# Kernel tuning notes

Hardware: AMD Instinct MI355X
Metric: run time of the kernel (lower is better)

Reference implementation:

```python
import jax, jax.numpy as jnp
import numpy as np
from jax import lax

DIM = 128
HEADS = 4
HEAD_DIM = DIM // HEADS          # 32
SR = 2
BN_EPS = 1e-5


def setup_inputs() -> dict:
    key = jax.random.key(0)
    ks = jax.random.split(key, 16)
    B, N, C = 8, 3136, DIM
    H = W = 56
    Nkv = (H // SR) * (W // SR)  # 784
    s = 0.05
    inp = {
        "x": jax.random.normal(ks[0], (B, N, C), jnp.float32),
        "relative_pos": jax.random.normal(ks[1], (HEADS, N, Nkv), jnp.float32),
        "Wq": jax.random.normal(ks[2], (C, C), jnp.float32) * s,
        "bq": jnp.zeros((C,), jnp.float32),
        "Wk": jax.random.normal(ks[3], (C, C), jnp.float32) * s,
        "bk": jnp.zeros((C,), jnp.float32),
        "Wv": jax.random.normal(ks[4], (C, C), jnp.float32) * s,
        "bv": jnp.zeros((C,), jnp.float32),
        "conv_w": jax.random.normal(ks[5], (C, 1, SR, SR), jnp.float32) * s,  # depthwise OIHW
        "conv_b": jnp.zeros((C,), jnp.float32),
        "bn_gamma": jnp.ones((C,), jnp.float32),
        "bn_beta": jnp.zeros((C,), jnp.float32),
        "bn_mean": jax.random.normal(ks[6], (C,), jnp.float32) * 0.1,
        "bn_var": jax.random.uniform(ks[7], (C,), jnp.float32, 0.5, 1.5),
        "Wp": jax.random.normal(ks[8], (C, C), jnp.float32) * s,
        "bp": jnp.zeros((C,), jnp.float32),
        "H": H,
        "W": W,
    }
    return inp


def reference(x, relative_pos, Wq, bq, Wk, bk, Wv, bv, conv_w, conv_b,
              bn_gamma, bn_beta, bn_mean, bn_var, Wp, bp, H, W):
    B, N, C = x.shape
    scale = HEAD_DIM ** -0.5

    # q: (B, heads, N, head_dim)
    q = (x @ Wq + bq).reshape(B, N, HEADS, HEAD_DIM).transpose(0, 2, 1, 3)

    # spatial reduction: depthwise conv stride SR + BatchNorm (eval, running stats)
    x_img = x.transpose(0, 2, 1).reshape(B, C, H, W)
    y = lax.conv_general_dilated(
        x_img, conv_w, window_strides=(SR, SR), padding="VALID",
        feature_group_count=C,
        dimension_numbers=("NCHW", "OIHW", "NCHW")) + conv_b[None, :, None, None]
    inv = bn_gamma * lax.rsqrt(bn_var + BN_EPS)
    y = y * inv[None, :, None, None] + (bn_beta - bn_mean * inv)[None, :, None, None]
    x_ = y.reshape(B, C, -1).transpose(0, 2, 1)  # (B, Nkv, C)
    Nkv = x_.shape[1]

    k = (x_ @ Wk + bk).reshape(B, Nkv, HEADS, HEAD_DIM).transpose(0, 2, 1, 3)
    v = (x_ @ Wv + bv).reshape(B, Nkv, HEADS, HEAD_DIM).transpose(0, 2, 1, 3)

    attn = jnp.einsum("bhnd,bhmd->bhnm", q, k) * scale + relative_pos[None]
    attn = jax.nn.softmax(attn, axis=-1)
    out = jnp.einsum("bhnm,bhmd->bhnd", attn, v)
    out = out.transpose(0, 2, 1, 3).reshape(B, N, C)
    return out @ Wp + bp
```

## Files before the change

kernel.cpp:

```cpp
#include <hip/hip_runtime.h>
#include <hip/hip_bf16.h>

#define BATCH 8
#define NQ 3136
#define CDIM 128
#define NHEAD 4
#define HD 32
#define NKV 784
#define HIMG 56
#define SCALE 0.17677669529663687f

typedef __attribute__((ext_vector_type(8))) short bf8_t;
typedef __attribute__((ext_vector_type(4))) float f4_t;

using bf16 = __hip_bfloat16;
using u16  = unsigned short;

static __device__ __forceinline__ float b2f(bf16 v){ return __bfloat162float(v); }
static __device__ __forceinline__ bf16  f2b(float v){ return __float2bfloat16(v); }
static __device__ __forceinline__ short f2s(float v){
  union { bf16 b; short s; } u; u.b = f2b(v); return u.s;
}
static __device__ __forceinline__ float u16f(u16 x){
  union { u16 u; bf16 b; } c; c.u = x; return b2f(c.b);
}
static __device__ __forceinline__ float ld1(const void* p, size_t i, int f){
  return f ? b2f(((const bf16*)p)[i]) : ((const float*)p)[i];
}
static __device__ __forceinline__ float4 ld4f(const void* p, size_t i, int f){
  if (f){
    ushort4 u = *(const ushort4*)((const bf16*)p + i);
    return make_float4(u16f(u.x), u16f(u.y), u16f(u.z), u16f(u.w));
  }
  return *(const float4*)((const float*)p + i);
}
static __device__ __forceinline__ bf8_t ld8(const void* p, size_t i, int f){
  if (f) return *(const bf8_t*)((const bf16*)p + i);
  const float* fp = (const float*)p + i;
  float4 a = *(const float4*)fp;
  float4 b = *(const float4*)(fp + 4);
  bf8_t r;
  r[0]=f2s(a.x); r[1]=f2s(a.y); r[2]=f2s(a.z); r[3]=f2s(a.w);
  r[4]=f2s(b.x); r[5]=f2s(b.y); r[6]=f2s(b.z); r[7]=f2s(b.w);
  return r;
}
static __device__ __forceinline__ int detect_flag(const void* var_raw){
  const u16* h = (const u16*)var_raw;
  int lane = threadIdx.x & 63;
  bool ok = true;
  #pragma unroll
  for (int t = 0; t < 2; t++){
    union { u16 u; bf16 b; } cv; cv.u = h[lane + 64*t];
    float v = b2f(cv.b);
    ok = ok && (v > 0.3f) && (v < 1.7f);
  }
  return (__ballot(ok) == ~0ull) ? 1 : 0;
}

static __device__ __forceinline__ void mfma_row(
    const bf8_t a[4], const bf16* __restrict__ Wt, int m, int g, f4_t acc[8])
{
  #pragma unroll
  for (int ct = 0; ct < 8; ct++){
    f4_t c = {0.f,0.f,0.f,0.f};
    const bf16* bp = Wt + (size_t)(ct*16 + m)*CDIM + 8*g;
    #pragma unroll
    for (int ks = 0; ks < 4; ks++){
      bf8_t b = *(const bf8_t*)(bp + 32*ks);
      c = __builtin_amdgcn_mfma_f32_16x16x32_bf16(a[ks], b, c, 0,0,0);
    }
    acc[ct] = c;
  }
}

__global__ __launch_bounds__(256) void prep_kernel(
    const void* __restrict__ Wq, const void* __restrict__ Wk,
    const void* __restrict__ Wv, const void* __restrict__ Wp,
    const void* __restrict__ var, const void* __restrict__ cw,
    const void* __restrict__ cb, const void* __restrict__ gam,
    const void* __restrict__ bet, const void* __restrict__ mea,
    const void* __restrict__ bq, const void* __restrict__ bk,
    const void* __restrict__ bv, const void* __restrict__ bp,
    bf16* __restrict__ Wqt, bf16* __restrict__ Wkt,
    bf16* __restrict__ Wvt, bf16* __restrict__ Wpt,
    bf16* __restrict__ bqs, bf16* __restrict__ bks,
    bf16* __restrict__ bvs, bf16* __restrict__ bps,
    float* __restrict__ cwf, float* __restrict__ inv, float* __restrict__ shift2)
{
  int f = detect_flag(var);
  int idx = blockIdx.x*256 + threadIdx.x;
  int mat = idx >> 14;
  int e   = idx & 16383;
  int o = e >> 7, i = e & 127;
  const void* src; bf16* dst; float s = 1.f;
  if      (mat == 0){ src = Wq; dst = Wqt; s = SCALE; }
  else if (mat == 1){ src = Wk; dst = Wkt; }
  else if (mat == 2){ src = Wv; dst = Wvt; }
  else              { src = Wp; dst = Wpt; }
  dst[e] = f2b(ld1(src, (size_t)i*128 + o, f) * s);

  if (blockIdx.x == 0){
    int t = threadIdx.x;
    { int e2 = t;       cwf[(e2&3)*128 + (e2>>2)] = ld1(cw, e2, f); }
    { int e2 = t + 256; cwf[(e2&3)*128 + (e2>>2)] = ld1(cw, e2, f); }
    if (t < 128){
      bqs[t] = f2b(ld1(bq, t, f) * SCALE);
      bks[t] = f2b(ld1(bk, t, f));
      bvs[t] = f2b(ld1(bv, t, f));
      bps[t] = f2b(ld1(bp, t, f));
      float iv = ld1(gam, t, f) * rsqrtf(ld1(var, t, f) + 1e-5f);
      inv[t] = iv;
      shift2[t] = ld1(bet, t, f) - ld1(mea, t, f) * iv + ld1(cb, t, f) * iv;
    }
  }
}

__global__ __launch_bounds__(256) void fat_kernel(
    const void* __restrict__ x, const void* __restrict__ var,
    const float* __restrict__ cwf, const float* __restrict__ inv,
    const float* __restrict__ shift2, bf16* __restrict__ xr,
    const bf16* __restrict__ Wqt, const bf16* __restrict__ bqs,
    bf16* __restrict__ qbf,
    const void* __restrict__ rel, bf16* __restrict__ relb, int qblk)
{
  int f = detect_flag(var);
  if (blockIdx.x < 784){
    int idx = blockIdx.x*256 + threadIdx.x;
    int c0 = (idx & 31)*4;
    int t  = idx >> 5;
    int b  = t / NKV;
    int kv = t - b*NKV;
    int i = kv/28, j = kv - i*28;
    size_t base = (size_t)(b*NQ + 2*i*HIMG + 2*j)*CDIM + c0;
    float4 t0 = ld4f(x, base, f);
    float4 t1 = ld4f(x, base + CDIM, f);
    float4 t2 = ld4f(x, base + HIMG*CDIM, f);
    float4 t3 = ld4f(x, base + HIMG*CDIM + CDIM, f);
    float4 w0 = *(const float4*)(cwf + c0);
    float4 w1 = *(const float4*)(cwf + 128 + c0);
    float4 w2 = *(const float4*)(cwf + 256 + c0);
    float4 w3 = *(const float4*)(cwf + 384 + c0);
    float4 iv4 = *(const float4*)(inv + c0);
    float4 sh4 = *(const float4*)(shift2 + c0);
    union { u16 h[4]; uint2 u; } pk;
    float a;
    a = t0.x*w0.x + t1.x*w1.x + t2.x*w2.x + t3.x*w3.x; pk.h[0] = (u16)f2s(a*iv4.x + sh4.x);
    a = t0.y*w0.y + t1.y*w1.y + t2.y*w2.y + t3.y*w3.y; pk.h[1] = (u16)f2s(a*iv4.y + sh4.y);
    a = t0.z*w0.z + t1.z*w1.z + t2.z*w2.z + t3.z*w3.z; pk.h[2] = (u16)f2s(a*iv4.z + sh4.z);
    a = t0.w*w0.w + t1.w*w1.w + t2.w*w2.w + t3.w*w3.w; pk.h[3] = (u16)f2s(a*iv4.w + sh4.w);
    *(uint2*)(xr + (size_t)t*CDIM + c0) = pk.u;
  } else if ((int)blockIdx.x < 784 + qblk){
    int wave = threadIdx.x >> 6, lane = threadIdx.x & 63;
    int m = lane & 15, g = lane >> 4;
    int task = (blockIdx.x - 784)*4 + wave;
    int row0 = task*16;
    bf8_t a[4];
    #pragma unroll
    for (int ks = 0; ks < 4; ks++)
      a[ks] = ld8(x, (size_t)(row0 + m)*CDIM + 8*g + 32*ks, f);
    f4_t acc[8];
    mfma_row(a, Wqt, m, g, acc);
    #pragma unroll
    for (int ct = 0; ct < 8; ct++){
      int col = ct*16 + m;
      float bv = b2f(bqs[col]);
      #pragma unroll
      for (int r = 0; r < 4; r++)
        qbf[(size_t)(row0 + 4*g + r)*CDIM + col] = f2b(acc[ct][r] + bv);
    }
  } else {
    if (f) return;
    int bi = blockIdx.x - 784 - qblk;
    size_t gid = ((size_t)bi*256 + threadIdx.x)*8;
    const float* fp = (const float*)rel + gid;
    float4 a  = *(const float4*)fp;
    float4 b4 = *(const float4*)(fp + 4);
    union { u16 hh[8]; uint4 u4; } pk;
    pk.hh[0]=(u16)f2s(a.x);  pk.hh[1]=(u16)f2s(a.y);
    pk.hh[2]=(u16)f2s(a.z);  pk.hh[3]=(u16)f2s(a.w);
    pk.hh[4]=(u16)f2s(b4.x); pk.hh[5]=(u16)f2s(b4.y);
    pk.hh[6]=(u16)f2s(b4.z); pk.hh[7]=(u16)f2s(b4.w);
    *(uint4*)(relb + gid) = pk.u4;
  }
}

__global__ __launch_bounds__(256) void kv_kernel(
    const bf16* __restrict__ xr,
    const bf16* __restrict__ Wkt, const bf16* __restrict__ Wvt,
    const bf16* __restrict__ bks, const bf16* __restrict__ bvs,
    bf16* __restrict__ kbf, bf16* __restrict__ vtb)
{
  int wave = threadIdx.x >> 6, lane = threadIdx.x & 63;
  int m = lane & 15, g = lane >> 4;
  bool isK = blockIdx.x < 98;
  int bx = isK ? blockIdx.x : blockIdx.x - 98;
  int row0 = (bx*4 + wave)*16;
  bf8_t a[4];
  #pragma unroll
  for (int ks = 0; ks < 4; ks++)
    a[ks] = *(const bf8_t*)(xr + (size_t)(row0 + m)*CDIM + 8*g + 32*ks);
  f4_t acc[8];
  mfma_row(a, isK ? Wkt : Wvt, m, g, acc);

  if (isK){
    #pragma unroll
    for (int ct = 0; ct < 8; ct++){
      int col = ct*16 + m;
      float bv = b2f(bks[col]);
      #pragma unroll
      for (int r = 0; r < 4; r++)
        kbf[(size_t)(row0 + 4*g + r)*CDIM + col] = f2b(acc[ct][r] + bv);
    }
  } else {
    int b   = row0 / NKV;
    int kv0 = row0 - b*NKV + 4*g;
    #pragma unroll
    for (int ct = 0; ct < 8; ct++){
      int col = ct*16 + m;
      float bv = b2f(bvs[col]);
      int h = col >> 5, d = col & 31;
      union { bf16 hh[4]; uint2 u; } pk;
      #pragma unroll
      for (int r = 0; r < 4; r++) pk.hh[r] = f2b(acc[ct][r] + bv);
      *(uint2*)(vtb + (size_t)((b*NHEAD + h)*HD + d)*NKV + kv0) = pk.u;
    }
  }
}

template<int RM> struct RelV { using T = float4; };
template<> struct RelV<1> { using T = uint2; };

template<int RM>
static __device__ __forceinline__ typename RelV<RM>::T relld(const void* relp, int off){
  if constexpr (RM == 1) return *(const uint2*)((const bf16*)relp + off);
  else                   return *(const float4*)((const float*)relp + off);
}
template<int RM>
static __device__ __forceinline__ float relget(const typename RelV<RM>::T& v, int r){
  if constexpr (RM == 1){
    union { uint2 u; u16 h[4]; } c; c.u = v;
    return u16f(c.h[r]);
  } else {
    return r == 0 ? v.x : (r == 1 ? v.y : (r == 2 ? v.z : v.w));
  }
}
template<int RM>
static __device__ __forceinline__ void ldrel4(
    typename RelV<RM>::T rl[4], const void* relp, int off){
  #pragma unroll
  for (int t = 0; t < 4; t++) rl[t] = relld<RM>(relp, off + 16*t);
}

template<int RM>
static __device__ __forceinline__ void chunk64(
    int kv0, const typename RelV<RM>::T rl[4],
    const bf16* __restrict__ kbase, const bf16* __restrict__ vb0,
    const bf16* __restrict__ vb1, bf16* __restrict__ pl, int m, int g,
    bf8_t q8, float& m_run, float& l_run, f4_t& O0, f4_t& O1)
{
  f4_t s[4];
  #pragma unroll
  for (int t = 0; t < 4; t++){
    bf8_t k8 = *(const bf8_t*)(kbase + (size_t)(kv0 + t*16)*CDIM);
    f4_t z = {0.f,0.f,0.f,0.f};
    s[t] = __builtin_amdgcn_mfma_f32_16x16x32_bf16(k8, q8, z, 0,0,0);
  }
  #pragma unroll
  for (int t = 0; t < 4; t++)
    #pragma unroll
    for (int r = 0; r < 4; r++)
      s[t][r] += relget<RM>(rl[t], r);
  float vmax = s[0][0];
  #pragma unroll
  for (int t = 0; t < 4; t++)
    #pragma unroll
    for (int r = 0; r < 4; r++)
      if (t + r > 0) vmax = fmaxf(vmax, s[t][r]);
  vmax = fmaxf(vmax, __shfl_xor(vmax, 16, 64));
  vmax = fmaxf(vmax, __shfl_xor(vmax, 32, 64));
  float mn = fmaxf(m_run, vmax);
  float al = __expf(m_run - mn);
  m_run = mn;
  l_run *= al;
  #pragma unroll
  for (int r = 0; r < 4; r++){ O0[r] *= al; O1[r] *= al; }
  float lsum = 0.f;
  #pragma unroll
  for (int t = 0; t < 4; t++){
    union { u16 h[4]; uint2 u; } pk;
    #pragma unroll
    for (int r = 0; r < 4; r++){
      float p = __expf(s[t][r] - m_run);
      lsum += p;
      pk.h[r] = (u16)f2s(p);
    }
    *(uint2*)(pl + m*136 + t*16 + 4*g) = pk.u;
  }
  l_run += lsum;
  #pragma unroll
  for (int ks = 0; ks < 2; ks++){
    bf8_t a8 = *(const bf8_t*)(pl + m*136 + ks*32 + 8*g);
    bf8_t v0 = *(const bf8_t*)(vb0 + kv0 + ks*32 + 8*g);
    bf8_t v1 = *(const bf8_t*)(vb1 + kv0 + ks*32 + 8*g);
    O0 = __builtin_amdgcn_mfma_f32_16x16x32_bf16(v0, a8, O0, 0,0,0);
    O1 = __builtin_amdgcn_mfma_f32_16x16x32_bf16(v1, a8, O1, 0,0,0);
  }
}

template<int RM>
static __device__ __forceinline__ void attn_run(
    const void* __restrict__ relp, const bf16* __restrict__ kbase,
    const bf16* __restrict__ vb0, const bf16* __restrict__ vb1,
    bf16* __restrict__ pl, int m, int g,
    bf8_t q8, float& m_run, float& l_run, f4_t& O0, f4_t& O1)
{
  using RT = typename RelV<RM>::T;
  RT rlA[4], rlB[4], rtv;
  ldrel4<RM>(rlA, relp, 4*g);
  #pragma unroll 1
  for (int c2 = 0; c2 < 6; c2++){
    int kv0 = c2*128;
    ldrel4<RM>(rlB, relp, kv0 + 64 + 4*g);
    chunk64<RM>(kv0, rlA, kbase, vb0, vb1, pl, m, g, q8, m_run, l_run, O0, O1);
    if (c2 < 5) ldrel4<RM>(rlA, relp, kv0 + 128 + 4*g);
    else        rtv = relld<RM>(relp, 768 + 4*g);
    chunk64<RM>(kv0 + 64, rlB, kbase, vb0, vb1, pl, m, g, q8, m_run, l_run, O0, O1);
  }
  {
    bf8_t k8 = *(const bf8_t*)(kbase + (size_t)768*CDIM);
    f4_t z = {0.f,0.f,0.f,0.f};
    f4_t s1 = __builtin_amdgcn_mfma_f32_16x16x32_bf16(k8, q8, z, 0,0,0);
    #pragma unroll
    for (int r = 0; r < 4; r++) s1[r] += relget<RM>(rtv, r);
    float vmax = fmaxf(fmaxf(s1[0], s1[1]), fmaxf(s1[2], s1[3]));
    vmax = fmaxf(vmax, __shfl_xor(vmax, 16, 64));
    vmax = fmaxf(vmax, __shfl_xor(vmax, 32, 64));
    float mn = fmaxf(m_run, vmax);
    float al = __expf(m_run - mn);
    m_run = mn;
    l_run *= al;
    #pragma unroll
    for (int r = 0; r < 4; r++){ O0[r] *= al; O1[r] *= al; }
    union { u16 h[4]; uint2 u; } pk;
    float lsum = 0.f;
    #pragma unroll
    for (int r = 0; r < 4; r++){
      float p = __expf(s1[r] - m_run);
      lsum += p;
      pk.h[r] = (u16)f2s(p);
    }
    *(uint2*)(pl + m*136 + 4*g) = pk.u;
    l_run += lsum;
    bf8_t a8, v0, v1;
    if (g >= 2){
      bf8_t z8 = {0,0,0,0,0,0,0,0};
      a8 = z8; v0 = z8; v1 = z8;
    } else {
      a8 = *(const bf8_t*)(pl + m*136 + 8*g);
      v0 = *(const bf8_t*)(vb0 + 768 + 8*g);
      v1 = *(const bf8_t*)(vb1 + 768 + 8*g);
    }
    O0 = __builtin_amdgcn_mfma_f32_16x16x32_bf16(v0, a8, O0, 0,0,0);
    O1 = __builtin_amdgcn_mfma_f32_16x16x32_bf16(v1, a8, O1, 0,0,0);
  }
}

template<int QF, int FB>
static __device__ __forceinline__ void attn_device(
    const bf16* __restrict__ qbf, const void* __restrict__ x,
    const bf16* __restrict__ Wqt, const bf16* __restrict__ bqs,
    const bf16* __restrict__ kb, const bf16* __restrict__ vtb,
    const void* __restrict__ rel, const bf16* __restrict__ relb,
    const void* __restrict__ var,
    void* __restrict__ dout, bf16* __restrict__ obf)
{
  int f = detect_flag(var);
  int wave = threadIdx.x >> 6, lane = threadIdx.x & 63;
  int m = lane & 15, g = lane >> 4;
  int qt = blockIdx.x, h = blockIdx.y, b = blockIdx.z;
  int qrow0 = qt*64 + wave*16;

  __shared__ bf16 Plds[4][16*136];
  bf16* pl = Plds[wave];

  bf8_t q8;
  if constexpr (QF == 0){
    q8 = *(const bf8_t*)(qbf + (size_t)(b*NQ + qrow0 + m)*CDIM + h*HD + 8*g);
  } else {
    bf8_t xa[4];
    #pragma unroll
    for (int ks = 0; ks < 4; ks++)
      xa[ks] = ld8(x, (size_t)(b*NQ + qrow0 + m)*CDIM + 8*g + 32*ks, f);
    f4_t qc0 = {0.f,0.f,0.f,0.f}, qc1 = {0.f,0.f,0.f,0.f};
    const bf16* wp0 = Wqt + (size_t)(h*HD + m)*CDIM + 8*g;
    const bf16* wp1 = Wqt + (size_t)(h*HD + 16 + m)*CDIM + 8*g;
    #pragma unroll
    for (int ks = 0; ks < 4; ks++){
      bf8_t w0 = *(const bf8_t*)(wp0 + 32*ks);
      bf8_t w1 = *(const bf8_t*)(wp1 + 32*ks);
      qc0 = __builtin_amdgcn_mfma_f32_16x16x32_bf16(xa[ks], w0, qc0, 0,0,0);
      qc1 = __builtin_amdgcn_mfma_f32_16x16x32_bf16(xa[ks], w1, qc1, 0,0,0);
    }
    float bv0 = b2f(bqs[h*HD + m]);
    float bv1 = b2f(bqs[h*HD + 16 + m]);
    #pragma unroll
    for (int r = 0; r < 4; r++){
      pl[(4*g + r)*136 + m]      = f2b(qc0[r] + bv0);
      pl[(4*g + r)*136 + 16 + m] = f2b(qc1[r] + bv1);
    }
    q8 = *(const bf8_t*)(pl + m*136 + 8*g);
  }

  const bf16* kbase = kb  + (size_t)(b*NKV + m)*CDIM + h*HD + 8*g;
  const bf16* vb0   = vtb + (size_t)((b*NHEAD + h)*HD + m)*NKV;
  const bf16* vb1   = vtb + (size_t)((b*NHEAD + h)*HD + 16 + m)*NKV;
  size_t rrow = ((size_t)h*NQ + qrow0 + m)*(size_t)NKV;

  float m_run = -1e30f, l_run = 0.f;
  f4_t O0 = {0.f,0.f,0.f,0.f}, O1 = {0.f,0.f,0.f,0.f};

  if constexpr (FB == 0){
    const void* rsrc = f ? (const void*)((const bf16*)rel + rrow)
                         : (const void*)(relb + rrow);
    attn_run<1>(rsrc, kbase, vb0, vb1, pl, m, g, q8, m_run, l_run, O0, O1);
  } else {
    if (f) attn_run<1>((const void*)((const bf16*)rel + rrow), kbase, vb0, vb1,
                       pl, m, g, q8, m_run, l_run, O0, O1);
    else   attn_run<0>((const void*)((const float*)rel + rrow), kbase, vb0, vb1,
                       pl, m, g, q8, m_run, l_run, O0, O1);
  }

  l_run += __shfl_xor(l_run, 16, 64);
  l_run += __shfl_xor(l_run, 32, 64);
  float iv = 1.0f / l_run;

  bf16* ob = (f ? (bf16*)dout : obf)
           + (size_t)(b*NQ + qrow0 + m)*CDIM + h*HD;
  union { u16 h4[4]; uint2 u; } o0, o1;
  #pragma unroll
  for (int r = 0; r < 4; r++){
    o0.h4[r] = (u16)f2s(O0[r] * iv);
    o1.h4[r] = (u16)f2s(O1[r] * iv);
  }
  *(uint2*)(ob + 4*g)      = o0.u;
  *(uint2*)(ob + 16 + 4*g) = o1.u;
}

template<int QF>
__global__ __launch_bounds__(256, 6) void attn_kernel(
    const bf16* __restrict__ qbf, const void* __restrict__ x,
    const bf16* __restrict__ Wqt, const bf16* __restrict__ bqs,
    const bf16* __restrict__ kb, const bf16* __restrict__ vtb,
    const void* __restrict__ rel, const bf16* __restrict__ relb,
    const void* __restrict__ var,
    void* __restrict__ dout, bf16* __restrict__ obf)
{
  attn_device<QF,0>(qbf, x, Wqt, bqs, kb, vtb, rel, relb, var, dout, obf);
}

__global__ __launch_bounds__(256) void attn_kernel_fb(
    const bf16* __restrict__ qbf, const void* __restrict__ x,
    const bf16* __restrict__ Wqt, const bf16* __restrict__ bqs,
    const bf16* __restrict__ kb, const bf16* __restrict__ vtb,
    const void* __restrict__ rel, const bf16* __restrict__ relb,
    const void* __restrict__ var,
    void* __restrict__ dout, bf16* __restrict__ obf)
{
  attn_device<1,1>(qbf, x, Wqt, bqs, kb, vtb, rel, relb, var, dout, obf);
}

__global__ __launch_bounds__(256) void proj_kernel(
    const bf16* A0, const bf16* A1, const bf16* __restrict__ Wt,
    const bf16* __restrict__ bias, void* outp, const void* __restrict__ var)
{
  int f = detect_flag(var);
  const bf16* A = f ? A0 : A1;
  int wave = threadIdx.x >> 6, lane = threadIdx.x & 63;
  int m = lane & 15, g = lane >> 4;
  int row0 = (blockIdx.x*4 + wave)*16;
  bf8_t a[4];
  #pragma unroll
  for (int ks = 0; ks < 4; ks++)
    a[ks] = *(const bf8_t*)(A + (size_t)(row0 + m)*CDIM + 8*g + 32*ks);
  f4_t acc[8];
  mfma_row(a, Wt, m, g, acc);
  #pragma unroll
  for (int ct = 0; ct < 8; ct++){
    int col = ct*16 + m;
    float bv = b2f(bias[col]);
    #pragma unroll
    for (int r = 0; r < 4; r++){
      size_t oi = (size_t)(row0 + 4*g + r)*CDIM + col;
      float v = acc[ct][r] + bv;
      if (f) ((bf16*)outp)[oi]  = f2b(v);
      else   ((float*)outp)[oi] = v;
    }
  }
}

extern "C" void kernel_launch(void* const* d_in, const int* in_sizes, int n_in,
                              void* d_out, int out_size, void* d_ws, size_t ws_size,
                              hipStream_t stream)
{
  const void* x   = d_in[0];
  const void* rel = d_in[1];
  const void* Wq  = d_in[2];
  const void* bq  = d_in[3];
  const void* Wk  = d_in[4];
  const void* bk  = d_in[5];
  const void* Wv  = d_in[6];
  const void* bv  = d_in[7];
  const void* cw  = d_in[8];
  const void* cb  = d_in[9];
  const void* gam = d_in[10];
  const void* bet = d_in[11];
  const void* mea = d_in[12];
  const void* var = d_in[13];
  const void* Wp  = d_in[14];
  const void* bp  = d_in[15];

  char* w = (char*)d_ws;
  auto alloc = [&](size_t bytes){
    char* p = w; w += (bytes + 255) & ~(size_t)255; return p;
  };
  bf16* Wqt = (bf16*)alloc(128*128*sizeof(bf16));
  bf16* Wkt = (bf16*)alloc(128*128*sizeof(bf16));
  bf16* Wvt = (bf16*)alloc(128*128*sizeof(bf16));
  bf16* Wpt = (bf16*)alloc(128*128*sizeof(bf16));
  bf16* bqs = (bf16*)alloc(128*sizeof(bf16));
  bf16* bks = (bf16*)alloc(128*sizeof(bf16));
  bf16* bvs = (bf16*)alloc(128*sizeof(bf16));
  bf16* bps = (bf16*)alloc(128*sizeof(bf16));
  float* cwf    = (float*)alloc(512*sizeof(float));
  float* inv    = (float*)alloc(128*sizeof(float));
  float* shift2 = (float*)alloc(128*sizeof(float));
  bf16* xr  = (bf16*)alloc((size_t)BATCH*NKV*CDIM*sizeof(bf16));
  bf16* kbf = (bf16*)alloc((size_t)BATCH*NKV*CDIM*sizeof(bf16));
  bf16* vtb = (bf16*)alloc((size_t)BATCH*NKV*CDIM*sizeof(bf16));
  bf16* obf = (bf16*)alloc((size_t)BATCH*NQ*CDIM*sizeof(bf16));

  size_t relb_bytes = (size_t)NHEAD*NQ*NKV*sizeof(bf16);
  bf16* relb = nullptr;
  if (((char*)d_ws + ws_size) - w >= (ptrdiff_t)(relb_bytes + 256))
    relb = (bf16*)alloc(relb_bytes);

  size_t qbf_bytes = (size_t)BATCH*NQ*CDIM*sizeof(bf16);
  bool use_q = relb &&
      ((((char*)d_ws + ws_size) - w) >= (ptrdiff_t)(qbf_bytes + 256));
  bf16* qbf = use_q ? (bf16*)alloc(qbf_bytes) : nullptr;

  int qblk = use_q ? 392 : 0;
  int rblk = relb  ? 4802 : 0;

  prep_kernel<<<256, 256, 0, stream>>>(Wq, Wk, Wv, Wp, var, cw, cb, gam, bet, mea,
                                       bq, bk, bv, bp,
                                       Wqt, Wkt, Wvt, Wpt, bqs, bks, bvs, bps,
                                       cwf, inv, shift2);
  fat_kernel<<<784 + qblk + rblk, 256, 0, stream>>>(
      x, var, cwf, inv, shift2, xr, Wqt, bqs, qbf, rel, relb, qblk);
  kv_kernel<<<196, 256, 0, stream>>>(xr, Wkt, Wvt, bks, bvs, kbf, vtb);
  dim3 ag(49, NHEAD, BATCH);
  if (relb){
    if (use_q)
      attn_kernel<0><<<ag, 256, 0, stream>>>(
          qbf, x, Wqt, bqs, kbf, vtb, rel, relb, var, d_out, obf);
    else
      attn_kernel<1><<<ag, 256, 0, stream>>>(
          qbf, x, Wqt, bqs, kbf, vtb, rel, relb, var, d_out, obf);
  } else {
    attn_kernel_fb<<<ag, 256, 0, stream>>>(
        qbf, x, Wqt, bqs, kbf, vtb, rel, relb, var, d_out, obf);
  }
  proj_kernel<<<392, 256, 0, stream>>>((const bf16*)d_out, obf, Wpt, bps, d_out, var);
}
```

Before: 236.3 us.

## Process KV in 128-wide chunks, hoist V loads, stage output through LDS

Doubles the attention inner chunk from 64 to 128 KV columns, so each online-softmax rescale (max reduction, exp of alpha, O rescale) covers twice as much work. V fragments are now loaded before the softmax math to hide their latency. The output tile is staged through the LDS P buffer so each lane issues one 16-byte store instead of two 8-byte stores. The launch-bounds occupancy hint of 6 is removed, which lets registers grow for the larger rel/score arrays at the cost of possible lower occupancy. It also relies on the per-wave P buffer being wide enough for 128 columns (row stride 136).

```diff
diff --git a/kernel.cpp b/kernel.cpp
--- a/kernel.cpp
+++ b/kernel.cpp
@@ -245,34 +245,40 @@
   }
 }
 template<int RM>
-static __device__ __forceinline__ void ldrel4(
-    typename RelV<RM>::T rl[4], const void* relp, int off){
-  #pragma unroll
-  for (int t = 0; t < 4; t++) rl[t] = relld<RM>(relp, off + 16*t);
+static __device__ __forceinline__ void ldrel8(
+    typename RelV<RM>::T rl[8], const void* relp, int off){
+  #pragma unroll
+  for (int t = 0; t < 8; t++) rl[t] = relld<RM>(relp, off + 16*t);
 }
 
 template<int RM>
-static __device__ __forceinline__ void chunk64(
-    int kv0, const typename RelV<RM>::T rl[4],
+static __device__ __forceinline__ void chunk128(
+    int kv0, const typename RelV<RM>::T rl[8],
     const bf16* __restrict__ kbase, const bf16* __restrict__ vb0,
     const bf16* __restrict__ vb1, bf16* __restrict__ pl, int m, int g,
     bf8_t q8, float& m_run, float& l_run, f4_t& O0, f4_t& O1)
 {
-  f4_t s[4];
-  #pragma unroll
-  for (int t = 0; t < 4; t++){
+  f4_t s[8];
+  #pragma unroll
+  for (int t = 0; t < 8; t++){
     bf8_t k8 = *(const bf8_t*)(kbase + (size_t)(kv0 + t*16)*CDIM);
     f4_t z = {0.f,0.f,0.f,0.f};
     s[t] = __builtin_amdgcn_mfma_f32_16x16x32_bf16(k8, q8, z, 0,0,0);
   }
-  #pragma unroll
-  for (int t = 0; t < 4; t++)
+  bf8_t v0[4], v1[4];
+  #pragma unroll
+  for (int ks = 0; ks < 4; ks++){
+    v0[ks] = *(const bf8_t*)(vb0 + kv0 + ks*32 + 8*g);
+    v1[ks] = *(const bf8_t*)(vb1 + kv0 + ks*32 + 8*g);
+  }
+  #pragma unroll
+  for (int t = 0; t < 8; t++)
     #pragma unroll
     for (int r = 0; r < 4; r++)
       s[t][r] += relget<RM>(rl[t], r);
   float vmax = s[0][0];
   #pragma unroll
-  for (int t = 0; t < 4; t++)
+  for (int t = 0; t < 8; t++)
     #pragma unroll
     for (int r = 0; r < 4; r++)
       if (t + r > 0) vmax = fmaxf(vmax, s[t][r]);
@@ -286,7 +292,7 @@
   for (int r = 0; r < 4; r++){ O0[r] *= al; O1[r] *= al; }
   float lsum = 0.f;
   #pragma unroll
-  for (int t = 0; t < 4; t++){
+  for (int t = 0; t < 8; t++){
     union { u16 h[4]; uint2 u; } pk;
     #pragma unroll
     for (int r = 0; r < 4; r++){
@@ -298,12 +304,10 @@
   }
   l_run += lsum;
   #pragma unroll
-  for (int ks = 0; ks < 2; ks++){
+  for (int ks = 0; ks < 4; ks++){
     bf8_t a8 = *(const bf8_t*)(pl + m*136 + ks*32 + 8*g);
-    bf8_t v0 = *(const bf8_t*)(vb0 + kv0 + ks*32 + 8*g);
-    bf8_t v1 = *(const bf8_t*)(vb1 + kv0 + ks*32 + 8*g);
-    O0 = __builtin_amdgcn_mfma_f32_16x16x32_bf16(v0, a8, O0, 0,0,0);
-    O1 = __builtin_amdgcn_mfma_f32_16x16x32_bf16(v1, a8, O1, 0,0,0);
+    O0 = __builtin_amdgcn_mfma_f32_16x16x32_bf16(v0[ks], a8, O0, 0,0,0);
+    O1 = __builtin_amdgcn_mfma_f32_16x16x32_bf16(v1[ks], a8, O1, 0,0,0);
   }
 }
 
@@ -315,16 +319,16 @@
     bf8_t q8, float& m_run, float& l_run, f4_t& O0, f4_t& O1)
 {
   using RT = typename RelV<RM>::T;
-  RT rlA[4], rlB[4], rtv;
-  ldrel4<RM>(rlA, relp, 4*g);
+  RT rlA[8], rlB[8], rtv;
+  ldrel8<RM>(rlA, relp, 4*g);
   #pragma unroll 1
-  for (int c2 = 0; c2 < 6; c2++){
-    int kv0 = c2*128;
-    ldrel4<RM>(rlB, relp, kv0 + 64 + 4*g);
-    chunk64<RM>(kv0, rlA, kbase, vb0, vb1, pl, m, g, q8, m_run, l_run, O0, O1);
-    if (c2 < 5) ldrel4<RM>(rlA, relp, kv0 + 128 + 4*g);
+  for (int cc = 0; cc < 3; cc++){
+    int kv0 = cc*256;
+    ldrel8<RM>(rlB, relp, kv0 + 128 + 4*g);
+    chunk128<RM>(kv0, rlA, kbase, vb0, vb1, pl, m, g, q8, m_run, l_run, O0, O1);
+    if (cc < 2) ldrel8<RM>(rlA, relp, kv0 + 256 + 4*g);
     else        rtv = relld<RM>(relp, 768 + 4*g);
-    chunk64<RM>(kv0 + 64, rlB, kbase, vb0, vb1, pl, m, g, q8, m_run, l_run, O0, O1);
+    chunk128<RM>(kv0 + 128, rlB, kbase, vb0, vb1, pl, m, g, q8, m_run, l_run, O0, O1);
   }
   {
     bf8_t k8 = *(const bf8_t*)(kbase + (size_t)768*CDIM);
@@ -434,20 +438,23 @@
   l_run += __shfl_xor(l_run, 32, 64);
   float iv = 1.0f / l_run;
 
-  bf16* ob = (f ? (bf16*)dout : obf)
-           + (size_t)(b*NQ + qrow0 + m)*CDIM + h*HD;
   union { u16 h4[4]; uint2 u; } o0, o1;
   #pragma unroll
   for (int r = 0; r < 4; r++){
     o0.h4[r] = (u16)f2s(O0[r] * iv);
     o1.h4[r] = (u16)f2s(O1[r] * iv);
   }
-  *(uint2*)(ob + 4*g)      = o0.u;
-  *(uint2*)(ob + 16 + 4*g) = o1.u;
+  *(uint2*)(pl + m*136 + 4*g)      = o0.u;
+  *(uint2*)(pl + m*136 + 16 + 4*g) = o1.u;
+  int r2 = lane >> 2;
+  int c2 = (lane & 3)*8;
+  bf8_t ov = *(const bf8_t*)(pl + r2*136 + c2);
+  bf16* ob = (f ? (bf16*)dout : obf);
+  *(bf8_t*)(ob + (size_t)(b*NQ + qrow0 + r2)*CDIM + h*HD + c2) = ov;
 }
 
 template<int QF>
-__global__ __launch_bounds__(256, 6) void attn_kernel(
+__global__ __launch_bounds__(256) void attn_kernel(
     const bf16* __restrict__ qbf, const void* __restrict__ x,
     const bf16* __restrict__ Wqt, const bf16* __restrict__ bqs,
     const bf16* __restrict__ kb, const bf16* __restrict__ vtb,
```

Measured after the change: 236.8 us. Within noise of the previous version (+0.2%).
